# Optimization experiments

Hardware: AMD Instinct MI355X
Metric: run time of the kernel (lower is better)

## Reference

```python
import jax, jax.numpy as jnp
import numpy as np

GRID_NUM = 28
IMG_SIZE = 224.0
GRID_SIZE = IMG_SIZE / GRID_NUM
LAMBDA_COORD = 5.0
LAMBDA_NOOBJ = 0.5
NUM_CLASSES = 20
EPS = 1e-12


def setup_inputs() -> dict:
    key = jax.random.key(0)
    k1, k2, k3 = jax.random.split(key, 3)
    B, S = 1024, GRID_NUM
    y_pred = jax.random.uniform(k1, (B, S, S, 30), dtype=jnp.float32)
    # y_true channel 0: class id in {0..20}; 0 means no object. channels 1:5: (x, y, w, h)
    cls = jax.random.randint(k2, (B, S, S, 1), 0, NUM_CLASSES + 1).astype(jnp.float32)
    box = jax.random.uniform(k3, (B, S, S, 4), dtype=jnp.float32)
    y_true = jnp.concatenate([cls, box], axis=-1)
    return {"y_pred": y_pred, "y_true": y_true}


def _corners(box, gi, gj):
    # box[..., 0:2] are cell-relative center offsets, box[..., 2:4] are image-relative w/h
    cx = (gj + box[..., 0]) * GRID_SIZE
    cy = (gi + box[..., 1]) * GRID_SIZE
    w = box[..., 2] * IMG_SIZE
    h = box[..., 3] * IMG_SIZE
    return cx - w / 2, cy - h / 2, cx + w / 2, cy + h / 2


def _iou(box_a, box_b, gi, gj):
    ax1, ay1, ax2, ay2 = _corners(box_a, gi, gj)
    bx1, by1, bx2, by2 = _corners(box_b, gi, gj)
    iw = jnp.maximum(jnp.minimum(ax2, bx2) - jnp.maximum(ax1, bx1), 0.0)
    ih = jnp.maximum(jnp.minimum(ay2, by2) - jnp.maximum(ay1, by1), 0.0)
    inter = iw * ih
    area_a = jnp.maximum(ax2 - ax1, 0.0) * jnp.maximum(ay2 - ay1, 0.0)
    area_b = jnp.maximum(bx2 - bx1, 0.0) * jnp.maximum(by2 - by1, 0.0)
    return inter / (area_a + area_b - inter + EPS)


def reference(y_pred, y_true):
    B, S = y_pred.shape[0], y_pred.shape[1]
    gi = jnp.arange(S, dtype=jnp.float32)[None, :, None]  # broadcast over (B, S, S)
    gj = jnp.arange(S, dtype=jnp.float32)[None, None, :]

    obj_mask = y_true[..., 0] != 0.0  # (B, S, S)
    true_box = y_true[..., 1:5]

    iou0 = _iou(y_pred[..., 0:4], true_box, gi, gj)
    iou1 = _iou(y_pred[..., 5:9], true_box, gi, gj)
    # original: choose 0 iff iou0 > iou1, else 1
    choose1 = ~(iou0 > iou1)

    conf_pred = jnp.where(choose1, y_pred[..., 9], y_pred[..., 4])
    conf_true = jnp.where(choose1, iou1, iou0)
    xy_pred = jnp.where(choose1[..., None], y_pred[..., 5:7], y_pred[..., 0:2])

    loss_conf_obj = jnp.square(conf_pred - conf_true)
    loss_coord = LAMBDA_COORD * jnp.sum(jnp.square(xy_pred - y_true[..., 1:3]), axis=-1)

    cls_idx = y_true[..., 0].astype(jnp.int32) - 1
    cls_onehot = jax.nn.one_hot(cls_idx, NUM_CLASSES, dtype=y_pred.dtype)
    loss_cls = jnp.sum(jnp.square(y_pred[..., 10:] - cls_onehot), axis=-1)

    loss_conf_noobj = LAMBDA_NOOBJ * (jnp.square(y_pred[..., 4]) + jnp.square(y_pred[..., 9]))

    bsz = jnp.float32(B)
    loss_confidence = jnp.sum(jnp.where(obj_mask, loss_conf_obj, loss_conf_noobj)) / bsz
    loss_coordinate = jnp.sum(jnp.where(obj_mask, loss_coord, 0.0)) / bsz
    loss_classification = jnp.sum(jnp.where(obj_mask, loss_cls, 0.0)) / bsz
    return loss_confidence + loss_coordinate + loss_classification
```

## Files before the change

### kernel.cpp

```cpp
#include <hip/hip_runtime.h>


#define S_GRID 28
#define N_CELLS (1024 * S_GRID * S_GRID)

__device__ __forceinline__ float iou_calc(float bx, float by, float bw, float bh,
                                          float tx, float ty, float tw, float th,
                                          float gi, float gj) {
    float acx = (gj + bx) * 8.0f;
    float acy = (gi + by) * 8.0f;
    float aw  = bw * 224.0f;
    float ah  = bh * 224.0f;
    float ax1 = acx - aw * 0.5f, ax2 = acx + aw * 0.5f;
    float ay1 = acy - ah * 0.5f, ay2 = acy + ah * 0.5f;
    float bcx = (gj + tx) * 8.0f;
    float bcy = (gi + ty) * 8.0f;
    float btw = tw * 224.0f;
    float bth = th * 224.0f;
    float bx1 = bcx - btw * 0.5f, bx2 = bcx + btw * 0.5f;
    float by1 = bcy - bth * 0.5f, by2 = bcy + bth * 0.5f;

    float iw = fmaxf(fminf(ax2, bx2) - fmaxf(ax1, bx1), 0.0f);
    float ih = fmaxf(fminf(ay2, by2) - fmaxf(ay1, by1), 0.0f);
    float inter = iw * ih;
    float area_a = fmaxf(ax2 - ax1, 0.0f) * fmaxf(ay2 - ay1, 0.0f);
    float area_b = fmaxf(bx2 - bx1, 0.0f) * fmaxf(by2 - by1, 0.0f);
    return inter / (area_a + area_b - inter + 1e-12f);
}

__global__ void zero_out_kernel(float* out) {
    out[0] = 0.0f;
}

__global__ __launch_bounds__(256) void yolo_loss_kernel(const float* __restrict__ y_pred,
                                                        const float* __restrict__ y_true,
                                                        float* __restrict__ out) {
    int c = blockIdx.x * blockDim.x + threadIdx.x;
    float val = 0.0f;
    if (c < N_CELLS) {
        int ij = c % (S_GRID * S_GRID);
        float gi = (float)(ij / S_GRID);
        float gj = (float)(ij % S_GRID);

        const float2* p2 = (const float2*)(y_pred + (size_t)c * 30);
        float pr[30];
#pragma unroll
        for (int k = 0; k < 15; ++k) {
            float2 v = p2[k];
            pr[2 * k]     = v.x;
            pr[2 * k + 1] = v.y;
        }
        const float* t = y_true + (size_t)c * 5;
        float tc = t[0], tx = t[1], ty = t[2], tw = t[3], th = t[4];

        float iou0 = iou_calc(pr[0], pr[1], pr[2], pr[3], tx, ty, tw, th, gi, gj);
        float iou1 = iou_calc(pr[5], pr[6], pr[7], pr[8], tx, ty, tw, th, gi, gj);
        bool choose1 = !(iou0 > iou1);

        float conf_pred = choose1 ? pr[9] : pr[4];
        float conf_true = choose1 ? iou1 : iou0;
        float xp = choose1 ? pr[5] : pr[0];
        float yp = choose1 ? pr[6] : pr[1];

        float dcf = conf_pred - conf_true;
        float loss_conf_obj = dcf * dcf;

        float d0 = xp - tx, d1 = yp - ty;
        float loss_coord = 5.0f * (d0 * d0 + d1 * d1);

        int cls = (int)tc - 1;
        float lcls = 0.0f;
#pragma unroll
        for (int k = 0; k < 20; ++k) {
            float oh = (k == cls) ? 1.0f : 0.0f;
            float d = pr[10 + k] - oh;
            lcls += d * d;
        }

        float loss_noobj = 0.5f * (pr[4] * pr[4] + pr[9] * pr[9]);

        bool obj = (tc != 0.0f);
        val = obj ? (loss_conf_obj + loss_coord + lcls) : loss_noobj;
    }

#pragma unroll
    for (int off = 32; off > 0; off >>= 1) {
        val += __shfl_down(val, off, 64);
    }
    __shared__ float wsum[4];
    int lane = threadIdx.x & 63;
    int wid  = threadIdx.x >> 6;
    if (lane == 0) wsum[wid] = val;
    __syncthreads();
    if (threadIdx.x == 0) {
        float s = wsum[0] + wsum[1] + wsum[2] + wsum[3];
        atomicAdd(out, s * (1.0f / 1024.0f));
    }
}

extern "C" void kernel_launch(void* const* d_in, const int* in_sizes, int n_in,
                              void* d_out, int out_size, void* d_ws, size_t ws_size,
                              hipStream_t stream) {
    const float* y_pred = (const float*)d_in[0];
    const float* y_true = (const float*)d_in[1];
    float* out = (float*)d_out;

    zero_out_kernel<<<1, 1, 0, stream>>>(out);
    int blocks = (N_CELLS + 255) / 256;
    yolo_loss_kernel<<<blocks, 256, 0, stream>>>(y_pred, y_true, out);
}
```

Before: 163.1 us.

## Stage inputs through shared memory with coalesced float4 loads

Each block cooperatively loads its 256 cells of predictions and targets into shared memory using contiguous float4 loads. Each thread then reads its own cell from LDS, with a padded stride of 31 to avoid bank conflicts. This replaces the strided per-thread global loads, which coalesced poorly. In exchange it uses about 37KB of LDS per block and adds a barrier, which may limit occupancy.

```diff
diff --git a/kernel.cpp b/kernel.cpp
--- a/kernel.cpp
+++ b/kernel.cpp
@@ -3,6 +3,7 @@
 
 #define S_GRID 28
 #define N_CELLS (1024 * S_GRID * S_GRID)
+#define CPB 256
 
 __device__ __forceinline__ float iou_calc(float bx, float by, float bw, float bh,
                                           float tx, float ty, float tw, float th,
@@ -32,67 +33,98 @@
     out[0] = 0.0f;
 }
 
-__global__ __launch_bounds__(256) void yolo_loss_kernel(const float* __restrict__ y_pred,
-                                                        const float* __restrict__ y_true,
+__global__ __launch_bounds__(256) void yolo_loss_kernel(const float4* __restrict__ yp4,
+                                                        const float4* __restrict__ yt4,
                                                         float* __restrict__ out) {
-    int c = blockIdx.x * blockDim.x + threadIdx.x;
-    float val = 0.0f;
-    if (c < N_CELLS) {
-        int ij = c % (S_GRID * S_GRID);
-        float gi = (float)(ij / S_GRID);
-        float gj = (float)(ij % S_GRID);
+    __shared__ float sp[CPB * 31];
+    __shared__ __align__(16) float st[CPB * 5];
 
-        const float2* p2 = (const float2*)(y_pred + (size_t)c * 30);
-        float pr[30];
+    int tid = threadIdx.x;
+    int bcell = blockIdx.x * CPB;
+
+    const float4* pb = yp4 + (size_t)blockIdx.x * (CPB * 30 / 4);
 #pragma unroll
-        for (int k = 0; k < 15; ++k) {
-            float2 v = p2[k];
-            pr[2 * k]     = v.x;
-            pr[2 * k + 1] = v.y;
+    for (int k = 0; k < 8; ++k) {
+        int idx = k * 256 + tid;
+        if (idx < 1920) {
+            float4 v = pb[idx];
+            int e = idx * 4;
+            float vals[4] = {v.x, v.y, v.z, v.w};
+#pragma unroll
+            for (int j = 0; j < 4; ++j) {
+                int ee = e + j;
+                int cell = ee / 30;
+                int rem = ee - cell * 30;
+                sp[cell * 31 + rem] = vals[j];
+            }
         }
-        const float* t = y_true + (size_t)c * 5;
-        float tc = t[0], tx = t[1], ty = t[2], tw = t[3], th = t[4];
+    }
 
-        float iou0 = iou_calc(pr[0], pr[1], pr[2], pr[3], tx, ty, tw, th, gi, gj);
-        float iou1 = iou_calc(pr[5], pr[6], pr[7], pr[8], tx, ty, tw, th, gi, gj);
-        bool choose1 = !(iou0 > iou1);
+    const float4* tb = yt4 + (size_t)blockIdx.x * (CPB * 5 / 4);
+#pragma unroll
+    for (int k = 0; k < 2; ++k) {
+        int idx = k * 256 + tid;
+        if (idx < 320) {
+            ((float4*)st)[idx] = tb[idx];
+        }
+    }
 
-        float conf_pred = choose1 ? pr[9] : pr[4];
-        float conf_true = choose1 ? iou1 : iou0;
-        float xp = choose1 ? pr[5] : pr[0];
-        float yp = choose1 ? pr[6] : pr[1];
+    __syncthreads();
 
-        float dcf = conf_pred - conf_true;
-        float loss_conf_obj = dcf * dcf;
+    int c = bcell + tid;
+    int ij = c % (S_GRID * S_GRID);
+    float gi = (float)(ij / S_GRID);
+    float gj = (float)(ij % S_GRID);
 
-        float d0 = xp - tx, d1 = yp - ty;
-        float loss_coord = 5.0f * (d0 * d0 + d1 * d1);
+    float pr[30];
+#pragma unroll
+    for (int k = 0; k < 30; ++k) pr[k] = sp[tid * 31 + k];
 
-        int cls = (int)tc - 1;
-        float lcls = 0.0f;
+    float tc = st[tid * 5 + 0];
+    float tx = st[tid * 5 + 1];
+    float ty = st[tid * 5 + 2];
+    float tw = st[tid * 5 + 3];
+    float th = st[tid * 5 + 4];
+
+    float iou0 = iou_calc(pr[0], pr[1], pr[2], pr[3], tx, ty, tw, th, gi, gj);
+    float iou1 = iou_calc(pr[5], pr[6], pr[7], pr[8], tx, ty, tw, th, gi, gj);
+    bool choose1 = !(iou0 > iou1);
+
+    float conf_pred = choose1 ? pr[9] : pr[4];
+    float conf_true = choose1 ? iou1 : iou0;
+    float xp = choose1 ? pr[5] : pr[0];
+    float yp = choose1 ? pr[6] : pr[1];
+
+    float dcf = conf_pred - conf_true;
+    float loss_conf_obj = dcf * dcf;
+
+    float d0 = xp - tx, d1 = yp - ty;
+    float loss_coord = 5.0f * (d0 * d0 + d1 * d1);
+
+    int cls = (int)tc - 1;
+    float lcls = 0.0f;
 #pragma unroll
-        for (int k = 0; k < 20; ++k) {
-            float oh = (k == cls) ? 1.0f : 0.0f;
-            float d = pr[10 + k] - oh;
-            lcls += d * d;
-        }
+    for (int k = 0; k < 20; ++k) {
+        float oh = (k == cls) ? 1.0f : 0.0f;
+        float d = pr[10 + k] - oh;
+        lcls += d * d;
+    }
 
-        float loss_noobj = 0.5f * (pr[4] * pr[4] + pr[9] * pr[9]);
+    float loss_noobj = 0.5f * (pr[4] * pr[4] + pr[9] * pr[9]);
 
-        bool obj = (tc != 0.0f);
-        val = obj ? (loss_conf_obj + loss_coord + lcls) : loss_noobj;
-    }
+    bool obj = (tc != 0.0f);
+    float val = obj ? (loss_conf_obj + loss_coord + lcls) : loss_noobj;
 
 #pragma unroll
     for (int off = 32; off > 0; off >>= 1) {
         val += __shfl_down(val, off, 64);
     }
     __shared__ float wsum[4];
-    int lane = threadIdx.x & 63;
-    int wid  = threadIdx.x >> 6;
+    int lane = tid & 63;
+    int wid  = tid >> 6;
     if (lane == 0) wsum[wid] = val;
     __syncthreads();
-    if (threadIdx.x == 0) {
+    if (tid == 0) {
         float s = wsum[0] + wsum[1] + wsum[2] + wsum[3];
         atomicAdd(out, s * (1.0f / 1024.0f));
     }
@@ -101,11 +133,11 @@
 extern "C" void kernel_launch(void* const* d_in, const int* in_sizes, int n_in,
                               void* d_out, int out_size, void* d_ws, size_t ws_size,
                               hipStream_t stream) {
-    const float* y_pred = (const float*)d_in[0];
-    const float* y_true = (const float*)d_in[1];
+    const float4* y_pred = (const float4*)d_in[0];
+    const float4* y_true = (const float4*)d_in[1];
     float* out = (float*)d_out;
 
     zero_out_kernel<<<1, 1, 0, stream>>>(out);
-    int blocks = (N_CELLS + 255) / 256;
+    int blocks = N_CELLS / CPB;
     yolo_loss_kernel<<<blocks, 256, 0, stream>>>(y_pred, y_true, out);
 }
```

New measurement: 175.4 us. +7.5%, slower.
